# Performance work log

Hardware: AMD Instinct MI355X
Metric: run time of the kernel (lower is better)

The kernel has to match this reference:

```python
import jax, jax.numpy as jnp
import numpy as np

NNZ = 524288
IN_FEATURES = 50000
OUT_FEATURES = 512
N_ROWS = 4096


def setup_inputs() -> dict:
    key = jax.random.key(0)
    k1, k2, k3, k4, k5 = jax.random.split(key, 5)
    values = jax.random.normal(k1, (NNZ,), dtype=jnp.float32)
    weight = jax.random.normal(k2, (IN_FEATURES, OUT_FEATURES), dtype=jnp.float32)
    bias = jax.random.normal(k3, (OUT_FEATURES,), dtype=jnp.float32)
    rows = jax.random.randint(k4, (NNZ,), 0, N_ROWS)
    cols = jax.random.randint(k5, (NNZ,), 0, IN_FEATURES)
    return {
        "values": values,
        "weight": weight,
        "bias": bias,
        "rows": rows,
        "cols": cols,
        "n_rows": N_ROWS,
    }


def reference(values, weight, bias, rows, cols, n_rows):
    # SpMM: out[r, :] = sum_{k: rows[k]==r} values[k] * weight[cols[k], :]
    contrib = values[:, None] * weight[cols]               # [nnz, out]
    out = jax.ops.segment_sum(contrib, rows, num_segments=n_rows)  # [n_rows, out]
    return out + bias
```

## Files before the change

kernel.cpp:

```cpp
#include <hip/hip_runtime.h>
#include <hip/hip_fp16.h>


struct Pair { int c; float v; };

__global__ void convert_count_kernel(const float* __restrict__ weight,
                                     __half* __restrict__ wf16, long long ngroups,
                                     const int* __restrict__ rows,
                                     int* __restrict__ counts, int nnz) {
    long long i = (long long)blockIdx.x * blockDim.x + threadIdx.x;
    if (i < nnz) atomicAdd(&counts[rows[(int)i]], 1);
    const float4* w4 = (const float4*)weight;
    float4* dst = (float4*)wf16;
    long long stride = (long long)gridDim.x * blockDim.x;
    for (long long g = i; g < ngroups; g += stride) {
        float4 a = w4[2 * g];
        float4 b = w4[2 * g + 1];
        union { __half2 h2[4]; float4 f4; } u;
        u.h2[0] = __floats2half2_rn(a.x, a.y);
        u.h2[1] = __floats2half2_rn(a.z, a.w);
        u.h2[2] = __floats2half2_rn(b.x, b.y);
        u.h2[3] = __floats2half2_rn(b.z, b.w);
        dst[g] = u.f4;
    }
}

__global__ void scan_kernel(const int* __restrict__ counts, int* __restrict__ offsets,
                            int* __restrict__ cursor, int n_rows) {
    __shared__ int partial[256];
    const int t = threadIdx.x;
    const int per = (n_rows + 255) / 256;
    const int base = t * per;
    int sum = 0;
    for (int j = 0; j < per; ++j) {
        int idx = base + j;
        if (idx < n_rows) sum += counts[idx];
    }
    partial[t] = sum;
    __syncthreads();
    for (int off = 1; off < 256; off <<= 1) {
        int v = 0;
        if (t >= off) v = partial[t - off];
        __syncthreads();
        if (t >= off) partial[t] += v;
        __syncthreads();
    }
    int run = (t == 0) ? 0 : partial[t - 1];
    for (int j = 0; j < per; ++j) {
        int idx = base + j;
        if (idx < n_rows) {
            offsets[idx] = run;
            cursor[idx] = run;
            run += counts[idx];
        }
    }
    if (t == 255) offsets[n_rows] = run;
}

__global__ void scatter_pairs_kernel(const int* __restrict__ rows, const int* __restrict__ cols,
                                     const float* __restrict__ values, int* __restrict__ cursor,
                                     int2* __restrict__ pairs, int nnz) {
    int i = blockIdx.x * blockDim.x + threadIdx.x;
    if (i < nnz) {
        int p = atomicAdd(&cursor[rows[i]], 1);
        pairs[p] = make_int2(cols[i], __float_as_int(values[i]));
    }
}

__global__ __launch_bounds__(256) void accum_f16_kernel(
    const __half* __restrict__ wf16, const float* __restrict__ bias,
    const int* __restrict__ offsets, const int2* __restrict__ pairs,
    float* __restrict__ out, int out_f) {
    const int wave = threadIdx.x >> 6;
    const int lane = threadIdx.x & 63;
    const int row = blockIdx.x;
    const int start = offsets[row];
    const int end = offsets[row + 1];
    const int len = end - start;
    const int per = (len + 3) >> 2;
    int p = start + wave * per;
    int pe = p + per;
    if (pe > end) pe = end;
    if (p > end) p = end;

    const float4* wbase = (const float4*)wf16;
    float acc[8] = {0.f, 0.f, 0.f, 0.f, 0.f, 0.f, 0.f, 0.f};

    for (; p + 4 <= pe; p += 4) {
        int2 e0 = pairs[p];
        int2 e1 = pairs[p + 1];
        int2 e2 = pairs[p + 2];
        int2 e3 = pairs[p + 3];
        float4 w0 = wbase[(long long)e0.x * 64 + lane];
        float4 w1 = wbase[(long long)e1.x * 64 + lane];
        float4 w2 = wbase[(long long)e2.x * 64 + lane];
        float4 w3 = wbase[(long long)e3.x * 64 + lane];
        float v0 = __int_as_float(e0.y);
        float v1 = __int_as_float(e1.y);
        float v2 = __int_as_float(e2.y);
        float v3 = __int_as_float(e3.y);
        const __half2* h0 = (const __half2*)&w0;
        const __half2* h1 = (const __half2*)&w1;
        const __half2* h2 = (const __half2*)&w2;
        const __half2* h3 = (const __half2*)&w3;
#pragma unroll
        for (int j = 0; j < 4; ++j) {
            float2 f0 = __half22float2(h0[j]);
            float2 f1 = __half22float2(h1[j]);
            float2 f2 = __half22float2(h2[j]);
            float2 f3 = __half22float2(h3[j]);
            acc[2 * j]     += v0 * f0.x + v1 * f1.x + v2 * f2.x + v3 * f3.x;
            acc[2 * j + 1] += v0 * f0.y + v1 * f1.y + v2 * f2.y + v3 * f3.y;
        }
    }
    for (; p < pe; ++p) {
        int2 e0 = pairs[p];
        float v0 = __int_as_float(e0.y);
        float4 w0 = wbase[(long long)e0.x * 64 + lane];
        const __half2* h0 = (const __half2*)&w0;
#pragma unroll
        for (int j = 0; j < 4; ++j) {
            float2 f0 = __half22float2(h0[j]);
            acc[2 * j]     += v0 * f0.x;
            acc[2 * j + 1] += v0 * f0.y;
        }
    }

    __shared__ float red[4][512];
    {
        float4* dst = (float4*)&red[wave][lane * 8];
        dst[0] = make_float4(acc[0], acc[1], acc[2], acc[3]);
        dst[1] = make_float4(acc[4], acc[5], acc[6], acc[7]);
    }
    __syncthreads();
    const int c = threadIdx.x * 2;
    float s0 = red[0][c] + red[1][c] + red[2][c] + red[3][c];
    float s1 = red[0][c + 1] + red[1][c + 1] + red[2][c + 1] + red[3][c + 1];
    float2 b = *(const float2*)(bias + c);
    *(float2*)(out + (long long)row * out_f + c) = make_float2(s0 + b.x, s1 + b.y);
}

__global__ void count_rows_kernel(const int* __restrict__ rows, int* __restrict__ counts, int nnz) {
    int i = blockIdx.x * blockDim.x + threadIdx.x;
    if (i < nnz) atomicAdd(&counts[rows[i]], 1);
}
__global__ void scatter_kernel(const int* __restrict__ rows, int* __restrict__ cursor,
                               int* __restrict__ perm, int nnz) {
    int i = blockIdx.x * blockDim.x + threadIdx.x;
    if (i < nnz) {
        int p = atomicAdd(&cursor[rows[i]], 1);
        perm[p] = i;
    }
}
__global__ void accum_kernel(const float* __restrict__ values, const float* __restrict__ weight,
                             const float* __restrict__ bias, const int* __restrict__ cols,
                             const int* __restrict__ offsets, const int* __restrict__ perm,
                             float* __restrict__ out, int out_f) {
    const int r = blockIdx.x;
    const int start = offsets[r];
    const int end = offsets[r + 1];
    const int step = blockDim.x * 4;
    for (int base = threadIdx.x * 4; base < out_f; base += step) {
        float4 acc = make_float4(0.f, 0.f, 0.f, 0.f);
        for (int p = start; p < end; ++p) {
            int k = perm[p];
            float v = values[k];
            long long c = cols[k];
            float4 w = *(const float4*)(weight + c * (long long)out_f + base);
            acc.x += v * w.x; acc.y += v * w.y; acc.z += v * w.z; acc.w += v * w.w;
        }
        float4 b = *(const float4*)(bias + base);
        acc.x += b.x; acc.y += b.y; acc.z += b.z; acc.w += b.w;
        *(float4*)(out + (long long)r * out_f + base) = acc;
    }
}

static size_t align_up(size_t x, size_t a) { return (x + a - 1) & ~(a - 1); }

extern "C" void kernel_launch(void* const* d_in, const int* in_sizes, int n_in,
                              void* d_out, int out_size, void* d_ws, size_t ws_size,
                              hipStream_t stream) {
    const float* values = (const float*)d_in[0];
    const float* weight = (const float*)d_in[1];
    const float* bias   = (const float*)d_in[2];
    const int*   rows   = (const int*)d_in[3];
    const int*   cols   = (const int*)d_in[4];

    const int nnz = in_sizes[0];
    const long long wtotal = in_sizes[1];
    const int out_f = in_sizes[2];
    const int n_rows = out_size / out_f;
    float* out = (float*)d_out;

    size_t off_wf16 = 0;
    size_t off_counts = align_up(off_wf16 + (size_t)wtotal * sizeof(__half), 256);
    size_t off_offsets = off_counts + (size_t)n_rows * sizeof(int);
    size_t off_cursor = off_offsets + (size_t)(n_rows + 1) * sizeof(int);
    size_t off_pairs = align_up(off_cursor + (size_t)n_rows * sizeof(int), 256);
    size_t need = off_pairs + (size_t)nnz * sizeof(int2);

    if (ws_size >= need && out_f == 512) {
        char* ws = (char*)d_ws;
        __half* wf16 = (__half*)(ws + off_wf16);
        int* counts = (int*)(ws + off_counts);
        int* offsets = (int*)(ws + off_offsets);
        int* cursor = (int*)(ws + off_cursor);
        int2* pairs = (int2*)(ws + off_pairs);

        hipMemsetAsync(counts, 0, (size_t)n_rows * sizeof(int), stream);

        long long ngroups = wtotal / 8;
        int cc_blocks = (int)((ngroups + 255) / 256);
        convert_count_kernel<<<cc_blocks, 256, 0, stream>>>(weight, wf16, ngroups,
                                                            rows, counts, nnz);
        scan_kernel<<<1, 256, 0, stream>>>(counts, offsets, cursor, n_rows);
        int sc_blocks = (nnz + 255) / 256;
        scatter_pairs_kernel<<<sc_blocks, 256, 0, stream>>>(rows, cols, values, cursor,
                                                            pairs, nnz);
        accum_f16_kernel<<<n_rows, 256, 0, stream>>>(wf16, bias, offsets, pairs,
                                                     out, out_f);
    } else {
        int* counts = (int*)d_ws;
        int* offsets = counts + n_rows;
        int* cursor = offsets + n_rows + 1;
        int* perm = cursor + n_rows;
        hipMemsetAsync(counts, 0, (size_t)n_rows * sizeof(int), stream);
        int blocks = (nnz + 255) / 256;
        count_rows_kernel<<<blocks, 256, 0, stream>>>(rows, counts, nnz);
        scan_kernel<<<1, 256, 0, stream>>>(counts, offsets, cursor, n_rows);
        scatter_kernel<<<blocks, 256, 0, stream>>>(rows, cursor, perm, nnz);
        accum_kernel<<<n_rows, 128, 0, stream>>>(values, weight, bias, cols,
                                                 offsets, perm, out, out_f);
    }
}
```

Measured before the change: 320.7 us.

## Vectorize preprocessing kernels and use nontemporal loads and stores

Each thread in the count and scatter kernels now handles four nonzeros through 128-bit loads of rows, cols and values. The fp16 weight conversion processes 16 floats per thread and writes with nontemporal stores. The scan kernel reads and writes counts and offsets with int4 vectors, and the accumulation kernel reads the (col, value) pairs with nontemporal loads. The aim is to cut memory-instruction count and cache pollution in the preprocessing stages, at the cost of a serial tail loop and a new divisibility guard on the fast path.

```diff
diff --git a/kernel.cpp b/kernel.cpp
--- a/kernel.cpp
+++ b/kernel.cpp
@@ -2,26 +2,46 @@
 #include <hip/hip_fp16.h>
 
 
-struct Pair { int c; float v; };
+typedef float f4v __attribute__((ext_vector_type(4)));
+typedef int   i4v __attribute__((ext_vector_type(4)));
+typedef int   i2v __attribute__((ext_vector_type(2)));
 
 __global__ void convert_count_kernel(const float* __restrict__ weight,
-                                     __half* __restrict__ wf16, long long ngroups,
+                                     __half* __restrict__ wf16, long long ngroups16,
                                      const int* __restrict__ rows,
                                      int* __restrict__ counts, int nnz) {
     long long i = (long long)blockIdx.x * blockDim.x + threadIdx.x;
-    if (i < nnz) atomicAdd(&counts[rows[(int)i]], 1);
-    const float4* w4 = (const float4*)weight;
-    float4* dst = (float4*)wf16;
+
+    int nquads = nnz >> 2;
+    if (i < nquads) {
+        i4v r = ((const i4v*)rows)[i];
+        atomicAdd(&counts[r.x], 1);
+        atomicAdd(&counts[r.y], 1);
+        atomicAdd(&counts[r.z], 1);
+        atomicAdd(&counts[r.w], 1);
+    } else if (i == nquads) {
+        for (int k = nquads * 4; k < nnz; ++k) atomicAdd(&counts[rows[k]], 1);
+    }
+
+    const f4v* w4 = (const f4v*)weight;
+    f4v* dst = (f4v*)wf16;
     long long stride = (long long)gridDim.x * blockDim.x;
-    for (long long g = i; g < ngroups; g += stride) {
-        float4 a = w4[2 * g];
-        float4 b = w4[2 * g + 1];
-        union { __half2 h2[4]; float4 f4; } u;
-        u.h2[0] = __floats2half2_rn(a.x, a.y);
-        u.h2[1] = __floats2half2_rn(a.z, a.w);
-        u.h2[2] = __floats2half2_rn(b.x, b.y);
-        u.h2[3] = __floats2half2_rn(b.z, b.w);
-        dst[g] = u.f4;
+    for (long long g = i; g < ngroups16; g += stride) {
+        f4v a = w4[4 * g + 0];
+        f4v b = w4[4 * g + 1];
+        f4v c = w4[4 * g + 2];
+        f4v d = w4[4 * g + 3];
+        union { __half2 h2[4]; f4v v; } u0, u1;
+        u0.h2[0] = __floats2half2_rn(a.x, a.y);
+        u0.h2[1] = __floats2half2_rn(a.z, a.w);
+        u0.h2[2] = __floats2half2_rn(b.x, b.y);
+        u0.h2[3] = __floats2half2_rn(b.z, b.w);
+        u1.h2[0] = __floats2half2_rn(c.x, c.y);
+        u1.h2[1] = __floats2half2_rn(c.z, c.w);
+        u1.h2[2] = __floats2half2_rn(d.x, d.y);
+        u1.h2[3] = __floats2half2_rn(d.z, d.w);
+        __builtin_nontemporal_store(u0.v, &dst[2 * g]);
+        __builtin_nontemporal_store(u1.v, &dst[2 * g + 1]);
     }
 }
 
@@ -31,10 +51,20 @@
     const int t = threadIdx.x;
     const int per = (n_rows + 255) / 256;
     const int base = t * per;
+    const bool vec = (base + per <= n_rows) && ((per & 3) == 0);
+
     int sum = 0;
-    for (int j = 0; j < per; ++j) {
-        int idx = base + j;
-        if (idx < n_rows) sum += counts[idx];
+    if (vec) {
+        const i4v* c4 = (const i4v*)(counts + base);
+        for (int j = 0; j < per / 4; ++j) {
+            i4v q = c4[j];
+            sum += q.x + q.y + q.z + q.w;
+        }
+    } else {
+        for (int j = 0; j < per; ++j) {
+            int idx = base + j;
+            if (idx < n_rows) sum += counts[idx];
+        }
     }
     partial[t] = sum;
     __syncthreads();
@@ -46,12 +76,28 @@
         __syncthreads();
     }
     int run = (t == 0) ? 0 : partial[t - 1];
-    for (int j = 0; j < per; ++j) {
-        int idx = base + j;
-        if (idx < n_rows) {
-            offsets[idx] = run;
-            cursor[idx] = run;
-            run += counts[idx];
+    if (vec) {
+        const i4v* c4 = (const i4v*)(counts + base);
+        i4v* o4 = (i4v*)(offsets + base);
+        i4v* u4 = (i4v*)(cursor + base);
+        for (int j = 0; j < per / 4; ++j) {
+            i4v q = c4[j];
+            i4v o;
+            o.x = run; run += q.x;
+            o.y = run; run += q.y;
+            o.z = run; run += q.z;
+            o.w = run; run += q.w;
+            o4[j] = o;
+            u4[j] = o;
+        }
+    } else {
+        for (int j = 0; j < per; ++j) {
+            int idx = base + j;
+            if (idx < n_rows) {
+                offsets[idx] = run;
+                cursor[idx] = run;
+                run += counts[idx];
+            }
         }
     }
     if (t == 255) offsets[n_rows] = run;
@@ -61,9 +107,24 @@
                                      const float* __restrict__ values, int* __restrict__ cursor,
                                      int2* __restrict__ pairs, int nnz) {
     int i = blockIdx.x * blockDim.x + threadIdx.x;
-    if (i < nnz) {
-        int p = atomicAdd(&cursor[rows[i]], 1);
-        pairs[p] = make_int2(cols[i], __float_as_int(values[i]));
+    int nquads = nnz >> 2;
+    if (i < nquads) {
+        i4v r = ((const i4v*)rows)[i];
+        i4v c = ((const i4v*)cols)[i];
+        f4v v = ((const f4v*)values)[i];
+        int p0 = atomicAdd(&cursor[r.x], 1);
+        pairs[p0] = make_int2(c.x, __float_as_int(v.x));
+        int p1 = atomicAdd(&cursor[r.y], 1);
+        pairs[p1] = make_int2(c.y, __float_as_int(v.y));
+        int p2 = atomicAdd(&cursor[r.z], 1);
+        pairs[p2] = make_int2(c.z, __float_as_int(v.z));
+        int p3 = atomicAdd(&cursor[r.w], 1);
+        pairs[p3] = make_int2(c.w, __float_as_int(v.w));
+    } else if (i == nquads) {
+        for (int k = nquads * 4; k < nnz; ++k) {
+            int p = atomicAdd(&cursor[rows[k]], 1);
+            pairs[p] = make_int2(cols[k], __float_as_int(values[k]));
+        }
     }
 }
 
@@ -83,18 +144,19 @@
     if (pe > end) pe = end;
     if (p > end) p = end;
 
-    const float4* wbase = (const float4*)wf16;
+    const f4v* wbase = (const f4v*)wf16;
+    const i2v* pbase = (const i2v*)pairs;
     float acc[8] = {0.f, 0.f, 0.f, 0.f, 0.f, 0.f, 0.f, 0.f};
 
     for (; p + 4 <= pe; p += 4) {
-        int2 e0 = pairs[p];
-        int2 e1 = pairs[p + 1];
-        int2 e2 = pairs[p + 2];
-        int2 e3 = pairs[p + 3];
-        float4 w0 = wbase[(long long)e0.x * 64 + lane];
-        float4 w1 = wbase[(long long)e1.x * 64 + lane];
-        float4 w2 = wbase[(long long)e2.x * 64 + lane];
-        float4 w3 = wbase[(long long)e3.x * 64 + lane];
+        i2v e0 = __builtin_nontemporal_load(pbase + p);
+        i2v e1 = __builtin_nontemporal_load(pbase + p + 1);
+        i2v e2 = __builtin_nontemporal_load(pbase + p + 2);
+        i2v e3 = __builtin_nontemporal_load(pbase + p + 3);
+        f4v w0 = wbase[(long long)e0.x * 64 + lane];
+        f4v w1 = wbase[(long long)e1.x * 64 + lane];
+        f4v w2 = wbase[(long long)e2.x * 64 + lane];
+        f4v w3 = wbase[(long long)e3.x * 64 + lane];
         float v0 = __int_as_float(e0.y);
         float v1 = __int_as_float(e1.y);
         float v2 = __int_as_float(e2.y);
@@ -114,9 +176,9 @@
         }
     }
     for (; p < pe; ++p) {
-        int2 e0 = pairs[p];
+        i2v e0 = __builtin_nontemporal_load(pbase + p);
         float v0 = __int_as_float(e0.y);
-        float4 w0 = wbase[(long long)e0.x * 64 + lane];
+        f4v w0 = wbase[(long long)e0.x * 64 + lane];
         const __half2* h0 = (const __half2*)&w0;
 #pragma unroll
         for (int j = 0; j < 4; ++j) {
@@ -128,9 +190,9 @@
 
     __shared__ float red[4][512];
     {
-        float4* dst = (float4*)&red[wave][lane * 8];
-        dst[0] = make_float4(acc[0], acc[1], acc[2], acc[3]);
-        dst[1] = make_float4(acc[4], acc[5], acc[6], acc[7]);
+        float4* dstp = (float4*)&red[wave][lane * 8];
+        dstp[0] = make_float4(acc[0], acc[1], acc[2], acc[3]);
+        dstp[1] = make_float4(acc[4], acc[5], acc[6], acc[7]);
     }
     __syncthreads();
     const int c = threadIdx.x * 2;
@@ -199,7 +261,7 @@
     size_t off_pairs = align_up(off_cursor + (size_t)n_rows * sizeof(int), 256);
     size_t need = off_pairs + (size_t)nnz * sizeof(int2);
 
-    if (ws_size >= need && out_f == 512) {
+    if (ws_size >= need && out_f == 512 && (wtotal % 16) == 0) {
         char* ws = (char*)d_ws;
         __half* wf16 = (__half*)(ws + off_wf16);
         int* counts = (int*)(ws + off_counts);
@@ -209,12 +271,14 @@
 
         hipMemsetAsync(counts, 0, (size_t)n_rows * sizeof(int), stream);
 
-        long long ngroups = wtotal / 8;
-        int cc_blocks = (int)((ngroups + 255) / 256);
-        convert_count_kernel<<<cc_blocks, 256, 0, stream>>>(weight, wf16, ngroups,
+        long long ngroups16 = wtotal / 16;
+        long long needed = (ngroups16 > (long long)(nnz / 4 + 1)) ? ngroups16
+                                                                  : (long long)(nnz / 4 + 1);
+        int cc_blocks = (int)((needed + 255) / 256);
+        convert_count_kernel<<<cc_blocks, 256, 0, stream>>>(weight, wf16, ngroups16,
                                                             rows, counts, nnz);
         scan_kernel<<<1, 256, 0, stream>>>(counts, offsets, cursor, n_rows);
-        int sc_blocks = (nnz + 255) / 256;
+        int sc_blocks = (nnz / 4 + 1 + 255) / 256;
         scatter_pairs_kernel<<<sc_blocks, 256, 0, stream>>>(rows, cols, values, cursor,
                                                             pairs, nnz);
         accum_f16_kernel<<<n_rows, 256, 0, stream>>>(wf16, bias, offsets, pairs,
```

Result: no change. 324.3 us (+1.1%).
